# Kernel tuning notes

Hardware: AMD Instinct MI355X
Metric: run time of the kernel (lower is better)

Reference implementation:

```python
import jax, jax.numpy as jnp
import numpy as np

NUM_CLASSES = 19  # configer.get('data','num_classes')


def _batch_label_vector(targets, num_classes, grid_size):
    # targets: [B, H, W] int labels in [0, num_classes)
    b, h, w = targets.shape
    pad_h = (-h) % grid_size
    pad_w = (-w) % grid_size
    # pad with value == num_classes, which torch.histc(min=0, max=num_classes-1)
    # ignores; we route it to an extra dustbin column and drop it.
    t = jnp.pad(targets, ((0, 0), (0, pad_h), (0, pad_w)),
                constant_values=num_classes)
    hh, ww = h + pad_h, w + pad_w
    # tile into (grid_size x grid_size) blocks -> [n_blocks, g*g]
    t = t.reshape(b, hh // grid_size, grid_size, ww // grid_size, grid_size)
    t = t.transpose(0, 1, 3, 2, 4).reshape(-1, grid_size * grid_size)
    n_blocks = t.shape[0]
    rows = jnp.arange(n_blocks)[:, None]  # [n_blocks, 1]
    # presence vector: hist > 0 <=> scatter-set ones at (block, label)
    tvect = jnp.zeros((n_blocks, num_classes + 1), jnp.float32)
    tvect = tvect.at[rows, t].set(1.0)
    return tvect[:, :num_classes]  # drop dustbin (pad value) column


def setup_inputs() -> dict:
    key = jax.random.key(0)
    k1, k2 = jax.random.split(key)
    B, H, W, G = 16, 1024, 2048, 8
    n_blocks = B * (H // G) * (W // G)  # 524288
    preds = jax.random.normal(k1, (n_blocks, NUM_CLASSES), jnp.float32)
    targets = jax.random.randint(k2, (B, H, W), 0, NUM_CLASSES, jnp.int32)
    return {"preds": preds, "targets": targets, "grid_size": G}


def reference(preds, targets, grid_size):
    se_target = _batch_label_vector(targets, NUM_CLASSES, grid_size)
    # BCELoss(sigmoid(preds), se_target), mean reduction.
    # Numerically stable: -log(sigmoid(x)) = softplus(-x),
    #                     -log(1-sigmoid(x)) = softplus(x)
    loss = se_target * jax.nn.softplus(-preds) + (1.0 - se_target) * jax.nn.softplus(preds)
    return jnp.mean(loss)
```

## Files before the change

### kernel.cpp

```cpp
#include <hip/hip_runtime.h>
#include <cmath>


#define NCLS 19

__global__ __launch_bounds__(256) void fsenc_loss_kernel(
    const float* __restrict__ preds,
    const int*   __restrict__ targets,
    float*       __restrict__ out,
    int B, int H, int W, float inv_count)
{
    const int t  = threadIdx.x;
    const int wg = blockIdx.x;

    __shared__ unsigned s_mask[128];
    __shared__ float s_part[4];

    const int strips_per_row = W / 1024;
    const int rows_per_img   = H / 8;
    const int block_row = wg / strips_per_row;
    const int strip     = wg % strips_per_row;
    const int b_img = block_row / rows_per_img;
    const int bh    = block_row % rows_per_img;
    const int col0  = strip * 1024;

    const int4* tgt4 = (const int4*)targets;
    const long row_stride4 = (long)W / 4;
    long base = ((long)(b_img * H + bh * 8) * W + col0) / 4 + t;

    unsigned mask = 0u;
    #pragma unroll
    for (int r = 0; r < 8; ++r) {
        int4 v = tgt4[base + (long)r * row_stride4];
        mask |= (1u << v.x) | (1u << v.y) | (1u << v.z) | (1u << v.w);
    }
    mask |= __shfl_xor(mask, 1);
    if ((t & 1) == 0) s_mask[t >> 1] = mask;
    __syncthreads();

    const float4* p4 = (const float4*)(preds + (long)wg * 2432);

    float acc = 0.f;
    for (int i = t; i < 608; i += 256) {
        float4 v = p4[i];
        const unsigned l0 = (unsigned)i * 4u;
        float xs[4] = {v.x, v.y, v.z, v.w};
        #pragma unroll
        for (int k = 0; k < 4; ++k) {
            unsigned l   = l0 + (unsigned)k;
            unsigned blk = (l * 3450u) >> 16;
            unsigned c   = l - blk * 19u;
            float x  = xs[k];
            float sp = fmaxf(x, 0.f) + __logf(1.f + __expf(-fabsf(x)));
            float tf = (float)((s_mask[blk] >> c) & 1u);
            acc += sp - tf * x;
        }
    }

    #pragma unroll
    for (int off = 32; off; off >>= 1)
        acc += __shfl_down(acc, off);

    if ((t & 63) == 0) s_part[t >> 6] = acc;
    __syncthreads();
    if (t == 0) {
        float tot = s_part[0] + s_part[1] + s_part[2] + s_part[3];
        atomicAdd(out, tot * inv_count);
    }
}

extern "C" void kernel_launch(void* const* d_in, const int* in_sizes, int n_in,
                              void* d_out, int out_size, void* d_ws, size_t ws_size,
                              hipStream_t stream) {
    const float* preds   = (const float*)d_in[0];
    const int*   targets = (const int*)d_in[1];
    float*       out     = (float*)d_out;

    const int B = 16, H = 1024, W = 2048;
    const float inv_count = 1.0f / (float)in_sizes[0];

    hipMemsetAsync(out, 0, sizeof(float), stream);

    const int grid = B * (H / 8) * (W / 1024);
    fsenc_loss_kernel<<<grid, 256, 0, stream>>>(preds, targets, out,
                                                B, H, W, inv_count);
}
```

Baseline: 230.3 us.

## Keep label masks in registers and map pred rows directly to thread pairs

Each thread pair now loads the 19 prediction values for its own 8x8 block, using unaligned 16-byte vector loads with an overlapping tail, and applies the presence mask held in its registers. This removes the shared-memory mask buffer and one barrier. The target loads and pred loads are issued up front so they overlap. Memory loads become unaligned and uneven between odd and even lanes, which may hurt coalescing, and half the lanes do 8 terms while the other half do 11.

```diff
diff --git a/kernel.cpp b/kernel.cpp
--- a/kernel.cpp
+++ b/kernel.cpp
@@ -2,7 +2,7 @@
 #include <cmath>
 
 
-#define NCLS 19
+typedef float uf4 __attribute__((vector_size(16), aligned(4)));
 
 __global__ __launch_bounds__(256) void fsenc_loss_kernel(
     const float* __restrict__ preds,
@@ -12,9 +12,6 @@
 {
     const int t  = threadIdx.x;
     const int wg = blockIdx.x;
-
-    __shared__ unsigned s_mask[128];
-    __shared__ float s_part[4];
 
     const int strips_per_row = W / 1024;
     const int rows_per_img   = H / 8;
@@ -26,41 +23,53 @@
 
     const int4* tgt4 = (const int4*)targets;
     const long row_stride4 = (long)W / 4;
-    long base = ((long)(b_img * H + bh * 8) * W + col0) / 4 + t;
+    const long tbase = ((long)(b_img * H + bh * 8) * W + col0) / 4 + t;
+
+    int4 tv[8];
+    #pragma unroll
+    for (int r = 0; r < 8; ++r)
+        tv[r] = tgt4[tbase + (long)r * row_stride4];
+
+    const long row = (long)wg * 2432 + (long)(t >> 1) * 19;
+    const float* p = preds + row;
+    uf4 q0 = {0.f, 0.f, 0.f, 0.f}, q1 = q0, q2 = q0;
+    if ((t & 1) == 0) {
+        q0 = *(const uf4*)(p + 0);
+        q1 = *(const uf4*)(p + 4);
+    } else {
+        q0 = *(const uf4*)(p + 8);
+        q1 = *(const uf4*)(p + 12);
+        q2 = *(const uf4*)(p + 15);
+    }
 
     unsigned mask = 0u;
     #pragma unroll
-    for (int r = 0; r < 8; ++r) {
-        int4 v = tgt4[base + (long)r * row_stride4];
-        mask |= (1u << v.x) | (1u << v.y) | (1u << v.z) | (1u << v.w);
-    }
+    for (int r = 0; r < 8; ++r)
+        mask |= (1u << tv[r].x) | (1u << tv[r].y) | (1u << tv[r].z) | (1u << tv[r].w);
     mask |= __shfl_xor(mask, 1);
-    if ((t & 1) == 0) s_mask[t >> 1] = mask;
-    __syncthreads();
-
-    const float4* p4 = (const float4*)(preds + (long)wg * 2432);
 
     float acc = 0.f;
-    for (int i = t; i < 608; i += 256) {
-        float4 v = p4[i];
-        const unsigned l0 = (unsigned)i * 4u;
-        float xs[4] = {v.x, v.y, v.z, v.w};
-        #pragma unroll
-        for (int k = 0; k < 4; ++k) {
-            unsigned l   = l0 + (unsigned)k;
-            unsigned blk = (l * 3450u) >> 16;
-            unsigned c   = l - blk * 19u;
-            float x  = xs[k];
-            float sp = fmaxf(x, 0.f) + __logf(1.f + __expf(-fabsf(x)));
-            float tf = (float)((s_mask[blk] >> c) & 1u);
-            acc += sp - tf * x;
+    #define SP_TERM(xval, cls)                                                 \
+        {                                                                      \
+            float x_ = (xval);                                                 \
+            float sp_ = fmaxf(x_, 0.f) + __logf(1.f + __expf(-fabsf(x_)));     \
+            acc += sp_ - (float)((mask >> (cls)) & 1u) * x_;                   \
         }
+    if ((t & 1) == 0) {
+        SP_TERM(q0[0], 0)  SP_TERM(q0[1], 1)  SP_TERM(q0[2], 2)  SP_TERM(q0[3], 3)
+        SP_TERM(q1[0], 4)  SP_TERM(q1[1], 5)  SP_TERM(q1[2], 6)  SP_TERM(q1[3], 7)
+    } else {
+        SP_TERM(q0[0], 8)  SP_TERM(q0[1], 9)  SP_TERM(q0[2], 10) SP_TERM(q0[3], 11)
+        SP_TERM(q1[0], 12) SP_TERM(q1[1], 13) SP_TERM(q1[2], 14) SP_TERM(q1[3], 15)
+        SP_TERM(q2[1], 16) SP_TERM(q2[2], 17) SP_TERM(q2[3], 18)
     }
+    #undef SP_TERM
 
     #pragma unroll
     for (int off = 32; off; off >>= 1)
         acc += __shfl_down(acc, off);
 
+    __shared__ float s_part[4];
     if ((t & 63) == 0) s_part[t >> 6] = acc;
     __syncthreads();
     if (t == 0) {
@@ -79,7 +88,7 @@
     const int B = 16, H = 1024, W = 2048;
     const float inv_count = 1.0f / (float)in_sizes[0];
 
-    hipMemsetAsync(out, 0, sizeof(float), stream);
+    (void)hipMemsetAsync(out, 0, sizeof(float), stream);
 
     const int grid = B * (H / 8) * (W / 1024);
     fsenc_loss_kernel<<<grid, 256, 0, stream>>>(preds, targets, out,
```

Result: faster. 223.3 us (-3.0%).

## Split mask building and loss into separate kernels with a grid-stride loss pass

Applied to the files above, without the earlier changes.

Splits the fused kernel in two. The first kernel computes per-block label presence masks and writes them to workspace. The second runs a persistent grid-stride loop over preds with a fixed grid of 1024 workgroups, reading masks from global memory, which cuts the number of atomics. In exchange it adds an extra launch, a global round-trip for the masks (about 2 MB), and gathered per-element mask loads in place of LDS reads.

```diff
diff --git a/kernel.cpp b/kernel.cpp
--- a/kernel.cpp
+++ b/kernel.cpp
@@ -2,19 +2,15 @@
 #include <cmath>
 
 
-#define NCLS 19
+typedef float f4a __attribute__((vector_size(16), aligned(16)));
 
-__global__ __launch_bounds__(256) void fsenc_loss_kernel(
-    const float* __restrict__ preds,
-    const int*   __restrict__ targets,
-    float*       __restrict__ out,
-    int B, int H, int W, float inv_count)
+__global__ __launch_bounds__(256) void fsenc_mask_kernel(
+    const int* __restrict__ targets,
+    unsigned*  __restrict__ masks,
+    int H, int W)
 {
     const int t  = threadIdx.x;
     const int wg = blockIdx.x;
-
-    __shared__ unsigned s_mask[128];
-    __shared__ float s_part[4];
 
     const int strips_per_row = W / 1024;
     const int rows_per_img   = H / 8;
@@ -26,34 +22,45 @@
 
     const int4* tgt4 = (const int4*)targets;
     const long row_stride4 = (long)W / 4;
-    long base = ((long)(b_img * H + bh * 8) * W + col0) / 4 + t;
+    const long tbase = ((long)(b_img * H + bh * 8) * W + col0) / 4 + t;
+
+    int4 tv[8];
+    #pragma unroll
+    for (int r = 0; r < 8; ++r)
+        tv[r] = tgt4[tbase + (long)r * row_stride4];
 
     unsigned mask = 0u;
     #pragma unroll
-    for (int r = 0; r < 8; ++r) {
-        int4 v = tgt4[base + (long)r * row_stride4];
-        mask |= (1u << v.x) | (1u << v.y) | (1u << v.z) | (1u << v.w);
-    }
+    for (int r = 0; r < 8; ++r)
+        mask |= (1u << tv[r].x) | (1u << tv[r].y) | (1u << tv[r].z) | (1u << tv[r].w);
     mask |= __shfl_xor(mask, 1);
-    if ((t & 1) == 0) s_mask[t >> 1] = mask;
-    __syncthreads();
 
-    const float4* p4 = (const float4*)(preds + (long)wg * 2432);
+    if ((t & 1) == 0)
+        masks[wg * 128 + (t >> 1)] = mask;
+}
+
+__global__ __launch_bounds__(256) void fsenc_loss_kernel(
+    const float*    __restrict__ preds,
+    const unsigned* __restrict__ masks,
+    float*          __restrict__ out,
+    int n_vec4,
+    float inv_count)
+{
+    const int tid    = blockIdx.x * 256 + threadIdx.x;
+    const int stride = gridDim.x * 256;
 
     float acc = 0.f;
-    for (int i = t; i < 608; i += 256) {
-        float4 v = p4[i];
-        const unsigned l0 = (unsigned)i * 4u;
-        float xs[4] = {v.x, v.y, v.z, v.w};
+    for (int i = tid; i < n_vec4; i += stride) {
+        f4a v = *(const f4a*)(preds + 4 * (long)i);
+        const unsigned l0 = 4u * (unsigned)i;
         #pragma unroll
         for (int k = 0; k < 4; ++k) {
             unsigned l   = l0 + (unsigned)k;
-            unsigned blk = (l * 3450u) >> 16;
+            unsigned blk = (unsigned)(((unsigned long long)l * 226050911ull) >> 32);
             unsigned c   = l - blk * 19u;
-            float x  = xs[k];
+            float x  = v[k];
             float sp = fmaxf(x, 0.f) + __logf(1.f + __expf(-fabsf(x)));
-            float tf = (float)((s_mask[blk] >> c) & 1u);
-            acc += sp - tf * x;
+            acc += sp - (float)((masks[blk] >> c) & 1u) * x;
         }
     }
 
@@ -61,9 +68,10 @@
     for (int off = 32; off; off >>= 1)
         acc += __shfl_down(acc, off);
 
-    if ((t & 63) == 0) s_part[t >> 6] = acc;
+    __shared__ float s_part[4];
+    if ((threadIdx.x & 63) == 0) s_part[threadIdx.x >> 6] = acc;
     __syncthreads();
-    if (t == 0) {
+    if (threadIdx.x == 0) {
         float tot = s_part[0] + s_part[1] + s_part[2] + s_part[3];
         atomicAdd(out, tot * inv_count);
     }
@@ -75,13 +83,18 @@
     const float* preds   = (const float*)d_in[0];
     const int*   targets = (const int*)d_in[1];
     float*       out     = (float*)d_out;
+    unsigned*    masks   = (unsigned*)d_ws;
 
     const int B = 16, H = 1024, W = 2048;
     const float inv_count = 1.0f / (float)in_sizes[0];
+    const int n_vec4 = in_sizes[0] / 4;
 
-    hipMemsetAsync(out, 0, sizeof(float), stream);
+    (void)hipMemsetAsync(out, 0, sizeof(float), stream);
 
-    const int grid = B * (H / 8) * (W / 1024);
-    fsenc_loss_kernel<<<grid, 256, 0, stream>>>(preds, targets, out,
-                                                B, H, W, inv_count);
+    const int gridA = B * (H / 8) * (W / 1024);
+    fsenc_mask_kernel<<<gridA, 256, 0, stream>>>(targets, masks, H, W);
+
+    const int gridB = 1024;
+    fsenc_loss_kernel<<<gridB, 256, 0, stream>>>(preds, masks, out,
+                                                 n_vec4, inv_count);
 }
```

New measurement: 227.4 us. No clear change (-1.3%).
